# Kernel tuning notes

Measured on AMD Instinct MI355X. Metric: run time of the kernel, lower is better.

The kernel has to match this reference:

```python
import jax, jax.numpy as jnp
import numpy as np

DECAY = 0.9
THRESHOLD = 1.0


def setup_inputs() -> dict:
    key = jax.random.key(0)
    k1, k2 = jax.random.split(key)
    B, T, I, N = 128, 512, 1024, 1024
    x = jax.random.normal(k1, (B, T, I), dtype=jnp.float32)
    weights = jax.random.uniform(k2, (N, I), dtype=jnp.float32)  # torch.rand init
    return {"x": x, "weights": weights}


def reference(x, weights):
    # x: [B, T, I], weights: [N, I]
    # Hoist the matmul out of the time loop: currents[t] == weights @ x[:, t, :].T
    currents = jnp.einsum("ni,bti->tnb", weights, x)  # [T, N, B]

    def step(mp, i_t):
        mp = DECAY * mp + i_t
        spike_mask = (mp >= THRESHOLD).astype(mp.dtype)
        mp = mp * (1.0 - spike_mask)  # reset fired neurons
        return mp, spike_mask

    mp0 = jnp.zeros((weights.shape[0], x.shape[0]), dtype=x.dtype)  # [N, B]
    _, masks = jax.lax.scan(step, mp0, currents)
    return masks.sum(axis=0)  # spikes: [N, B]
```

## Files before the change

kernel.cpp:

```cpp
#include <hip/hip_runtime.h>
#include <stdint.h>

#define T_DIM 512
#define B_DIM 128
#define I_DIM 1024
#define N_DIM 1024
#define NB (N_DIM * B_DIM)
#define ROWB 4096

#define DECAY 0.9f
#define THRESH 1.0f

typedef _Float16 f16;
typedef _Float16 f16x8 __attribute__((ext_vector_type(8)));
typedef float f32x4 __attribute__((ext_vector_type(4)));

__global__ __launch_bounds__(256) void split_w_kernel(
    const float* __restrict__ W, f16* __restrict__ Ws)
{
    int gid = blockIdx.x * 256 + threadIdx.x;
    int kc  = gid & 127;
    int row = gid >> 7;
    const float* src = W + (size_t)row * I_DIM + kc * 8;
    f16* dst = Ws + (size_t)row * 2048 + kc * 16;
    float v[8];
    *(float4*)&v[0] = *(const float4*)src;
    *(float4*)&v[4] = *(const float4*)(src + 4);
    f16 hi[8], lo[8];
    #pragma unroll
    for (int j = 0; j < 8; ++j) {
        hi[j] = (f16)v[j];
        lo[j] = (f16)(v[j] - (float)hi[j]);
    }
    *(f16x8*)dst       = *(const f16x8*)hi;
    *(f16x8*)(dst + 8) = *(const f16x8*)lo;
}

__global__ __launch_bounds__(256, 2) void spk_gemm_kernel(
    const uint8_t* __restrict__ Wsb,
    const float* __restrict__ X,
    float* __restrict__ C,
    int t0)
{
    __shared__ __align__(16) uint8_t lds[65536];

    const int tid  = threadIdx.x;
    const int wave = tid >> 6, lane = tid & 63;

    const int nwg = gridDim.x;
    const int q = nwg >> 3, r = nwg & 7;
    const int xcd = blockIdx.x & 7, idx = blockIdx.x >> 3;
    const int wg = (xcd < r ? xcd * (q + 1) : r * (q + 1) + (xcd - r) * q) + idx;
    const int n0 = (wg & 7) << 7;
    const int t  = t0 + (wg >> 3);

    const uint8_t* srcp[8];
    #pragma unroll
    for (int c = 0; c < 8; ++c) {
        if (c < 4) {
            int G = c * 256 + tid;
            int rr = G >> 3, g = G & 7;
            srcp[c] = Wsb + (size_t)(n0 + rr) * ROWB + ((g ^ (rr & 7)) << 4);
        } else {
            int G = (c - 4) * 256 + tid;
            int rr = G >> 3, g = G & 7;
            srcp[c] = (const uint8_t*)X + ((size_t)rr * T_DIM + t) * (I_DIM * 4)
                      + ((g ^ (rr & 7)) << 4);
        }
    }

    const int wr = ((wave >> 1) << 6);
    const int wc = ((wave & 1) << 6);
    const int l15 = lane & 15, kcg = lane >> 4, l7 = l15 & 7;

    int aoffH[4], aoffL[4], boff0[4], boff1[4];
    #pragma unroll
    for (int m = 0; m < 4; ++m) {
        int ra = wr + m * 16 + l15;
        aoffH[m] = ra * 128 + ((((kcg << 1) | 0) ^ l7) << 4);
        aoffL[m] = ra * 128 + ((((kcg << 1) | 1) ^ l7) << 4);
        int rb = wc + m * 16 + l15;
        boff0[m] = 16384 + rb * 128 + (((kcg * 2 + 0) ^ l7) << 4);
        boff1[m] = 16384 + rb * 128 + (((kcg * 2 + 1) ^ l7) << 4);
    }

    f32x4 acc[4][4];
    #pragma unroll
    for (int m = 0; m < 4; ++m)
        #pragma unroll
        for (int n = 0; n < 4; ++n) acc[m][n] = (f32x4){0.f, 0.f, 0.f, 0.f};

    #pragma unroll
    for (int c = 0; c < 8; ++c)
        __builtin_amdgcn_global_load_lds(
            (const __attribute__((address_space(1))) uint8_t*)srcp[c],
            (__attribute__((address_space(3))) uint8_t*)&lds[(c * 256 + tid - lane) * 16],
            16, 0, 0);

    for (int kt = 0; kt < 32; ++kt) {
        const int buf = kt & 1;
        __builtin_amdgcn_s_barrier();
        if (kt + 1 < 32) {
            const int nb = (buf ^ 1) << 15;
            #pragma unroll
            for (int c = 0; c < 8; ++c)
                __builtin_amdgcn_global_load_lds(
                    (const __attribute__((address_space(1))) uint8_t*)(srcp[c] + (kt + 1) * 128),
                    (__attribute__((address_space(3))) uint8_t*)&lds[nb + (c * 256 + tid - lane) * 16],
                    16, 0, 0);
            asm volatile("s_waitcnt vmcnt(8)" ::: "memory");
        } else {
            asm volatile("s_waitcnt vmcnt(0)" ::: "memory");
        }
        __builtin_amdgcn_s_barrier();
        __builtin_amdgcn_sched_barrier(0);

        const uint8_t* bp = &lds[buf << 15];

        f32x4 b0[4], b1[4];
        #pragma unroll
        for (int n = 0; n < 4; ++n) {
            b0[n] = *(const f32x4*)&bp[boff0[n]];
            b1[n] = *(const f32x4*)&bp[boff1[n]];
        }
        f16x8 Ah[4], Al[4];
        #pragma unroll
        for (int m = 0; m < 4; ++m) {
            Ah[m] = *(const f16x8*)&bp[aoffH[m]];
            Al[m] = *(const f16x8*)&bp[aoffL[m]];
        }
        f16x8 Bh[4], Bl[4];
        #pragma unroll
        for (int n = 0; n < 4; ++n) {
            float bf[8];
            bf[0] = b0[n][0]; bf[1] = b0[n][1]; bf[2] = b0[n][2]; bf[3] = b0[n][3];
            bf[4] = b1[n][0]; bf[5] = b1[n][1]; bf[6] = b1[n][2]; bf[7] = b1[n][3];
            #pragma unroll
            for (int j = 0; j < 8; ++j) {
                f16 h = (f16)bf[j];
                Bh[n][j] = h;
                Bl[n][j] = (f16)(bf[j] - (float)h);
            }
        }

        __builtin_amdgcn_s_setprio(1);
        #pragma unroll
        for (int m = 0; m < 4; ++m)
            #pragma unroll
            for (int n = 0; n < 4; ++n)
                acc[m][n] = __builtin_amdgcn_mfma_f32_16x16x32_f16(Ah[m], Bh[n], acc[m][n], 0, 0, 0);
        #pragma unroll
        for (int m = 0; m < 4; ++m)
            #pragma unroll
            for (int n = 0; n < 4; ++n)
                acc[m][n] = __builtin_amdgcn_mfma_f32_16x16x32_f16(Ah[m], Bl[n], acc[m][n], 0, 0, 0);
        #pragma unroll
        for (int m = 0; m < 4; ++m)
            #pragma unroll
            for (int n = 0; n < 4; ++n)
                acc[m][n] = __builtin_amdgcn_mfma_f32_16x16x32_f16(Al[m], Bh[n], acc[m][n], 0, 0, 0);
        __builtin_amdgcn_s_setprio(0);
    }

    float* cp = C + (size_t)(wg >> 3) * NB;
    const int rg = (lane >> 4) << 2;
    #pragma unroll
    for (int m = 0; m < 4; ++m) {
        int nrow = n0 + wr + m * 16 + rg;
        #pragma unroll
        for (int n = 0; n < 4; ++n) {
            int col = wc + n * 16 + l15;
            #pragma unroll
            for (int j = 0; j < 4; ++j)
                cp[(size_t)(nrow + j) * B_DIM + col] = acc[m][n][j];
        }
    }
}

__global__ __launch_bounds__(256) void spk_scan_kernel(
    const float* __restrict__ cur,
    float* __restrict__ mp_state,
    float* __restrict__ out,
    int tc, int first)
{
    const int nb = blockIdx.x * 256 + threadIdx.x;
    float mp, cnt;
    if (first) { mp = 0.0f; cnt = 0.0f; }
    else       { mp = mp_state[nb]; cnt = out[nb]; }

    const float* p = cur + nb;
    #pragma unroll 8
    for (int t = 0; t < tc; ++t) {
        float c = p[(size_t)t * NB];
        mp = __fadd_rn(__fmul_rn(DECAY, mp), c);
        if (mp >= THRESH) { cnt += 1.0f; mp = 0.0f; }
    }
    mp_state[nb] = mp;
    out[nb] = cnt;
}

extern "C" void kernel_launch(void* const* d_in, const int* in_sizes, int n_in,
                              void* d_out, int out_size, void* d_ws, size_t ws_size,
                              hipStream_t stream) {
    const float* x = (const float*)d_in[0];
    const float* w = (const float*)d_in[1];
    float* out = (float*)d_out;

    uint8_t* ws = (uint8_t*)d_ws;
    float* mp  = (float*)ws;
    f16*   Wsp = (f16*)(ws + 524288);
    uint8_t* rest = ws + 524288 + 4194304;
    size_t rem = ws_size - 524288 - 4194304;

    int Tc = (int)(rem / (size_t)(NB * 4));
    if (Tc > T_DIM) Tc = T_DIM;
    if (Tc < 1) Tc = 1;

    float* cur = (float*)rest;

    split_w_kernel<<<(N_DIM * I_DIM / 8) / 256, 256, 0, stream>>>(w, Wsp);

    int first = 1;
    for (int t0 = 0; t0 < T_DIM; ) {
        int tc = T_DIM - t0;
        if (tc > Tc) tc = Tc;

        spk_gemm_kernel<<<tc * 8, 256, 0, stream>>>((const uint8_t*)Wsp, x, cur, t0);
        spk_scan_kernel<<<NB / 256, 256, 0, stream>>>(cur, mp, out, tc, first);

        first = 0;
        t0 += tc;
    }
}
```

Baseline: 528.0 us.

## Split X into f16 hi/lo once at staging with register-prefetched B pipeline

The X tile is now loaded from global memory into registers two k-steps ahead. It is converted once per tile into f16 hi/lo halves and written to swizzled LDS, so the compute phase reads ready-made f16 fragments for both operands. Before, each wave read fp32 B from LDS and redid the hi/lo split on its own fragments, which duplicated conversion work across waves sharing a column block. The loop is unrolled by two with explicit vmcnt/lgkmcnt waits to overlap A's async LDS loads, B's register loads and the conversion. In exchange, the kernel holds more registers for the staged B data, which could reduce occupancy, and relies on hand-counted waitcnt values.

```diff
diff --git a/kernel.cpp b/kernel.cpp
--- a/kernel.cpp
+++ b/kernel.cpp
@@ -14,6 +14,8 @@
 typedef _Float16 f16;
 typedef _Float16 f16x8 __attribute__((ext_vector_type(8)));
 typedef float f32x4 __attribute__((ext_vector_type(4)));
+
+struct B4 { float4 a, b, c, d; };
 
 __global__ __launch_bounds__(256) void split_w_kernel(
     const float* __restrict__ W, f16* __restrict__ Ws)
@@ -46,6 +48,7 @@
 
     const int tid  = threadIdx.x;
     const int wave = tid >> 6, lane = tid & 63;
+    const int wbase = wave << 6;
 
     const int nwg = gridDim.x;
     const int q = nwg >> 3, r = nwg & 7;
@@ -54,34 +57,34 @@
     const int n0 = (wg & 7) << 7;
     const int t  = t0 + (wg >> 3);
 
-    const uint8_t* srcp[8];
-    #pragma unroll
-    for (int c = 0; c < 8; ++c) {
-        if (c < 4) {
-            int G = c * 256 + tid;
-            int rr = G >> 3, g = G & 7;
-            srcp[c] = Wsb + (size_t)(n0 + rr) * ROWB + ((g ^ (rr & 7)) << 4);
-        } else {
-            int G = (c - 4) * 256 + tid;
-            int rr = G >> 3, g = G & 7;
-            srcp[c] = (const uint8_t*)X + ((size_t)rr * T_DIM + t) * (I_DIM * 4)
-                      + ((g ^ (rr & 7)) << 4);
-        }
-    }
+    const uint8_t* srcA[4];
+    #pragma unroll
+    for (int c = 0; c < 4; ++c) {
+        int G = c * 256 + tid;
+        int rr = G >> 3, g = G & 7;
+        srcA[c] = Wsb + (size_t)(n0 + rr) * ROWB + ((g ^ (rr & 7)) << 4);
+    }
+
+    const int brr = tid >> 1, bhh = tid & 1;
+    const uint8_t* bsrc = (const uint8_t*)X
+        + ((size_t)brr * T_DIM + t) * (I_DIM * 4) + bhh * 64;
+    const int dswH0 = 16384 + brr * 128 + (((bhh * 4 + 0) ^ (brr & 7)) << 4);
+    const int dswL0 = 16384 + brr * 128 + (((bhh * 4 + 1) ^ (brr & 7)) << 4);
+    const int dswH1 = 16384 + brr * 128 + (((bhh * 4 + 2) ^ (brr & 7)) << 4);
+    const int dswL1 = 16384 + brr * 128 + (((bhh * 4 + 3) ^ (brr & 7)) << 4);
 
     const int wr = ((wave >> 1) << 6);
     const int wc = ((wave & 1) << 6);
     const int l15 = lane & 15, kcg = lane >> 4, l7 = l15 & 7;
-
-    int aoffH[4], aoffL[4], boff0[4], boff1[4];
+    int aoffH[4], aoffL[4], boffH[4], boffL[4];
     #pragma unroll
     for (int m = 0; m < 4; ++m) {
         int ra = wr + m * 16 + l15;
         aoffH[m] = ra * 128 + ((((kcg << 1) | 0) ^ l7) << 4);
         aoffL[m] = ra * 128 + ((((kcg << 1) | 1) ^ l7) << 4);
         int rb = wc + m * 16 + l15;
-        boff0[m] = 16384 + rb * 128 + (((kcg * 2 + 0) ^ l7) << 4);
-        boff1[m] = 16384 + rb * 128 + (((kcg * 2 + 1) ^ l7) << 4);
+        boffH[m] = 16384 + rb * 128 + ((((kcg << 1) | 0) ^ l7) << 4);
+        boffL[m] = 16384 + rb * 128 + ((((kcg << 1) | 1) ^ l7) << 4);
     }
 
     f32x4 acc[4][4];
@@ -90,77 +93,106 @@
         #pragma unroll
         for (int n = 0; n < 4; ++n) acc[m][n] = (f32x4){0.f, 0.f, 0.f, 0.f};
 
-    #pragma unroll
-    for (int c = 0; c < 8; ++c)
-        __builtin_amdgcn_global_load_lds(
-            (const __attribute__((address_space(1))) uint8_t*)srcp[c],
-            (__attribute__((address_space(3))) uint8_t*)&lds[(c * 256 + tid - lane) * 16],
-            16, 0, 0);
-
-    for (int kt = 0; kt < 32; ++kt) {
-        const int buf = kt & 1;
-        __builtin_amdgcn_s_barrier();
-        if (kt + 1 < 32) {
-            const int nb = (buf ^ 1) << 15;
-            #pragma unroll
-            for (int c = 0; c < 8; ++c)
-                __builtin_amdgcn_global_load_lds(
-                    (const __attribute__((address_space(1))) uint8_t*)(srcp[c] + (kt + 1) * 128),
-                    (__attribute__((address_space(3))) uint8_t*)&lds[nb + (c * 256 + tid - lane) * 16],
-                    16, 0, 0);
-            asm volatile("s_waitcnt vmcnt(8)" ::: "memory");
-        } else {
-            asm volatile("s_waitcnt vmcnt(0)" ::: "memory");
-        }
-        __builtin_amdgcn_s_barrier();
-        __builtin_amdgcn_sched_barrier(0);
-
-        const uint8_t* bp = &lds[buf << 15];
-
-        f32x4 b0[4], b1[4];
-        #pragma unroll
-        for (int n = 0; n < 4; ++n) {
-            b0[n] = *(const f32x4*)&bp[boff0[n]];
-            b1[n] = *(const f32x4*)&bp[boff1[n]];
-        }
-        f16x8 Ah[4], Al[4];
-        #pragma unroll
-        for (int m = 0; m < 4; ++m) {
-            Ah[m] = *(const f16x8*)&bp[aoffH[m]];
-            Al[m] = *(const f16x8*)&bp[aoffL[m]];
-        }
-        f16x8 Bh[4], Bl[4];
-        #pragma unroll
-        for (int n = 0; n < 4; ++n) {
-            float bf[8];
-            bf[0] = b0[n][0]; bf[1] = b0[n][1]; bf[2] = b0[n][2]; bf[3] = b0[n][3];
-            bf[4] = b1[n][0]; bf[5] = b1[n][1]; bf[6] = b1[n][2]; bf[7] = b1[n][3];
-            #pragma unroll
-            for (int j = 0; j < 8; ++j) {
-                f16 h = (f16)bf[j];
-                Bh[n][j] = h;
-                Bl[n][j] = (f16)(bf[j] - (float)h);
-            }
-        }
-
-        __builtin_amdgcn_s_setprio(1);
-        #pragma unroll
-        for (int m = 0; m < 4; ++m)
-            #pragma unroll
-            for (int n = 0; n < 4; ++n)
-                acc[m][n] = __builtin_amdgcn_mfma_f32_16x16x32_f16(Ah[m], Bh[n], acc[m][n], 0, 0, 0);
-        #pragma unroll
-        for (int m = 0; m < 4; ++m)
-            #pragma unroll
-            for (int n = 0; n < 4; ++n)
-                acc[m][n] = __builtin_amdgcn_mfma_f32_16x16x32_f16(Ah[m], Bl[n], acc[m][n], 0, 0, 0);
-        #pragma unroll
-        for (int m = 0; m < 4; ++m)
-            #pragma unroll
-            for (int n = 0; n < 4; ++n)
-                acc[m][n] = __builtin_amdgcn_mfma_f32_16x16x32_f16(Al[m], Bh[n], acc[m][n], 0, 0, 0);
-        __builtin_amdgcn_s_setprio(0);
-    }
+#define STAGE_A(KT1, QB) do {                                                 \
+    _Pragma("unroll")                                                         \
+    for (int c_ = 0; c_ < 4; ++c_)                                            \
+        __builtin_amdgcn_global_load_lds(                                     \
+            (const __attribute__((address_space(1))) uint8_t*)(srcA[c_] + (KT1) * 128), \
+            (__attribute__((address_space(3))) uint8_t*)&lds[(QB) + (c_ * 256 + wbase) * 16], \
+            16, 0, 0);                                                        \
+} while (0)
+
+#define LOAD_B(KT2, SLD) do {                                                 \
+    const uint8_t* p_ = bsrc + (KT2) * 128;                                   \
+    (SLD).a = *(const float4*)(p_);                                           \
+    (SLD).b = *(const float4*)(p_ + 16);                                      \
+    (SLD).c = *(const float4*)(p_ + 32);                                      \
+    (SLD).d = *(const float4*)(p_ + 48);                                      \
+} while (0)
+
+#define CONV_WRITE(QB, SCV) do {                                              \
+    float bf_[16];                                                            \
+    *(float4*)&bf_[0]  = (SCV).a; *(float4*)&bf_[4]  = (SCV).b;               \
+    *(float4*)&bf_[8]  = (SCV).c; *(float4*)&bf_[12] = (SCV).d;               \
+    f16 h0_[8], l0_[8], h1_[8], l1_[8];                                       \
+    _Pragma("unroll")                                                         \
+    for (int j_ = 0; j_ < 8; ++j_) {                                          \
+        f16 h_ = (f16)bf_[j_];                                                \
+        h0_[j_] = h_; l0_[j_] = (f16)(bf_[j_] - (float)h_);                   \
+    }                                                                         \
+    _Pragma("unroll")                                                         \
+    for (int j_ = 0; j_ < 8; ++j_) {                                          \
+        f16 h_ = (f16)bf_[8 + j_];                                            \
+        h1_[j_] = h_; l1_[j_] = (f16)(bf_[8 + j_] - (float)h_);               \
+    }                                                                         \
+    *(f16x8*)&lds[(QB) + dswH0] = *(f16x8*)h0_;                               \
+    *(f16x8*)&lds[(QB) + dswL0] = *(f16x8*)l0_;                               \
+    *(f16x8*)&lds[(QB) + dswH1] = *(f16x8*)h1_;                               \
+    *(f16x8*)&lds[(QB) + dswL1] = *(f16x8*)l1_;                               \
+} while (0)
+
+#define COMPUTE(PB) do {                                                      \
+    const uint8_t* bp_ = &lds[(PB)];                                          \
+    f16x8 Ah_[4], Al_[4], Bh_[4], Bl_[4];                                     \
+    _Pragma("unroll")                                                         \
+    for (int m_ = 0; m_ < 4; ++m_) {                                          \
+        Ah_[m_] = *(const f16x8*)&bp_[aoffH[m_]];                             \
+        Al_[m_] = *(const f16x8*)&bp_[aoffL[m_]];                             \
+    }                                                                         \
+    _Pragma("unroll")                                                         \
+    for (int n_ = 0; n_ < 4; ++n_) {                                          \
+        Bh_[n_] = *(const f16x8*)&bp_[boffH[n_]];                             \
+        Bl_[n_] = *(const f16x8*)&bp_[boffL[n_]];                             \
+    }                                                                         \
+    __builtin_amdgcn_s_setprio(1);                                            \
+    _Pragma("unroll")                                                         \
+    for (int m_ = 0; m_ < 4; ++m_)                                            \
+        _Pragma("unroll")                                                     \
+        for (int n_ = 0; n_ < 4; ++n_)                                        \
+            acc[m_][n_] = __builtin_amdgcn_mfma_f32_16x16x32_f16(Ah_[m_], Bh_[n_], acc[m_][n_], 0, 0, 0); \
+    _Pragma("unroll")                                                         \
+    for (int m_ = 0; m_ < 4; ++m_)                                            \
+        _Pragma("unroll")                                                     \
+        for (int n_ = 0; n_ < 4; ++n_)                                        \
+            acc[m_][n_] = __builtin_amdgcn_mfma_f32_16x16x32_f16(Ah_[m_], Bl_[n_], acc[m_][n_], 0, 0, 0); \
+    _Pragma("unroll")                                                         \
+    for (int m_ = 0; m_ < 4; ++m_)                                            \
+        _Pragma("unroll")                                                     \
+        for (int n_ = 0; n_ < 4; ++n_)                                        \
+            acc[m_][n_] = __builtin_amdgcn_mfma_f32_16x16x32_f16(Al_[m_], Bh_[n_], acc[m_][n_], 0, 0, 0); \
+    __builtin_amdgcn_s_setprio(0);                                            \
+} while (0)
+
+#define ITER(KT, SLD, SCV, VMC, DOA, DOB, DOCV) do {                          \
+    __builtin_amdgcn_s_barrier();                 \
+    {                                                                         \
+        const int qb_ = ((((KT) & 1) ^ 1) << 15);                             \
+        if (DOA) STAGE_A((KT) + 1, qb_);                                      \
+        if (DOB) LOAD_B((KT) + 2, SLD);                                       \
+        asm volatile("s_waitcnt vmcnt(" #VMC ")" ::: "memory");               \
+        if (DOCV) {                                                           \
+            CONV_WRITE(qb_, SCV);                                             \
+            asm volatile("s_waitcnt lgkmcnt(0)" ::: "memory");                \
+        }                                                                     \
+        __builtin_amdgcn_s_barrier();             \
+        __builtin_amdgcn_sched_barrier(0);                                    \
+        COMPUTE(((KT) & 1) << 15);                                            \
+    }                                                                         \
+} while (0)
+
+    B4 sB0, sB1;
+    LOAD_B(0, sB0);
+    STAGE_A(0, 0);
+    LOAD_B(1, sB1);
+    CONV_WRITE(0, sB0);
+    asm volatile("s_waitcnt lgkmcnt(0)" ::: "memory");
+
+    for (int kt = 0; kt < 30; kt += 2) {
+        ITER(kt,     sB0, sB1, 8, 1, 1, 1);
+        ITER(kt + 1, sB1, sB0, 8, 1, 1, 1);
+    }
+    ITER(30, sB0, sB1, 4, 1, 0, 1);
+    ITER(31, sB1, sB0, 0, 0, 0, 0);
 
     float* cp = C + (size_t)(wg >> 3) * NB;
     const int rg = (lane >> 4) << 2;
```

New measurement: 683.6 us. 1.29x slower.
